# Performance work log

Measured on AMD Instinct MI355X. Metric: run time of the kernel, lower is better.

The kernel has to match this reference:

```python
import jax, jax.numpy as jnp
import numpy as np

N_NODES = 50000
DIM = 64
HEADS = 4
N_EDGES = 800000
NEG_SLOPE = 0.2  # PyG GATConv default


def setup_inputs() -> dict:
    key = jax.random.key(0)
    ks = jax.random.split(key, 8)
    H, C = HEADS, DIM
    embedding = jax.random.normal(ks[0], (N_NODES, DIM), dtype=jnp.float32)
    graph = jax.random.randint(ks[1], (2, N_EDGES), 0, N_NODES, dtype=jnp.int64)
    s = 1.0 / np.sqrt(DIM)
    # GATConv params: shared source/target linear (PyG uses one lin when in_channels is int)
    W = jax.random.normal(ks[2], (DIM, H * C), dtype=jnp.float32) * s
    att_src = jax.random.normal(ks[3], (H, C), dtype=jnp.float32) * s
    att_dst = jax.random.normal(ks[4], (H, C), dtype=jnp.float32) * s
    bias = jnp.zeros((H * C,), dtype=jnp.float32)
    # dense: Linear(dim*heads -> dim)
    dense_w = jax.random.normal(ks[5], (H * C, DIM), dtype=jnp.float32) / np.sqrt(H * C)
    dense_b = jnp.zeros((DIM,), dtype=jnp.float32)
    return {"embedding": embedding, "graph": graph, "W": W, "att_src": att_src,
            "att_dst": att_dst, "bias": bias, "dense_w": dense_w, "dense_b": dense_b}


def reference(embedding, graph, W, att_src, att_dst, bias, dense_w, dense_b):
    N, D = embedding.shape
    H, C = att_src.shape
    # linear projection, per-head view: [N, H, C]
    x = (embedding @ W).reshape(N, H, C)
    # add self loops (PyG default add_self_loops=True)
    ar = jnp.arange(N, dtype=graph.dtype)
    src = jnp.concatenate([graph[0], ar])  # [E+N]
    dst = jnp.concatenate([graph[1], ar])
    # per-node attention logits, gathered per edge
    a_src = jnp.einsum('nhc,hc->nh', x, att_src)  # [N, H]
    a_dst = jnp.einsum('nhc,hc->nh', x, att_dst)
    alpha = jax.nn.leaky_relu(a_src[src] + a_dst[dst], NEG_SLOPE)  # [E, H]
    # segment softmax over destination nodes
    amax = jax.ops.segment_max(alpha, dst, num_segments=N)  # [N, H]
    amax = jnp.where(jnp.isfinite(amax), amax, 0.0)
    ex = jnp.exp(alpha - amax[dst])
    denom = jax.ops.segment_sum(ex, dst, num_segments=N)
    coef = ex / (denom[dst] + 1e-16)  # [E, H]
    # weighted scatter-aggregate of source features
    msg = x[src] * coef[:, :, None]  # [E, H, C]
    agg = jax.ops.segment_sum(msg, dst, num_segments=N)  # [N, H, C]
    gat_out = agg.reshape(N, H * C) + bias  # concat heads + bias
    return gat_out @ dense_w + dense_b  # [N, D]
```

## Files before the change

### kernel.cpp

```cpp
#include <hip/hip_runtime.h>
#include <hip/hip_fp16.h>
#include <cfloat>
#include <cmath>

#define DIM 64
#define HEADS 4
#define NEG 0.2f
#define CAP 64

__device__ __forceinline__ float lrelu(float a) { return a > 0.0f ? a : NEG * a; }

__device__ __forceinline__ unsigned pack_half2(float a, float b) {
    return (unsigned)__half_as_ushort(__float2half(a)) |
           ((unsigned)__half_as_ushort(__float2half(b)) << 16);
}

__global__ __launch_bounds__(256) void prep_kernel(
        const float* __restrict__ W, const float* __restrict__ dw,
        const float* __restrict__ att_s, const float* __restrict__ att_d,
        const float* __restrict__ bias, const float* __restrict__ db,
        const float* __restrict__ emb,
        float* __restrict__ M, float* __restrict__ bvec,
        float* __restrict__ a_src, float* __restrict__ a_dst,
        float* __restrict__ pself, int* __restrict__ cnt, int N) {
    const int b = blockIdx.x, t = threadIdx.x;
    if (b < 64) {
        __shared__ float s_W[256];
        s_W[t] = W[b * 256 + t];
        __syncthreads();
        const int h = t >> 6, j = t & 63;
        float s = 0.f;
        for (int c = 0; c < 64; c++)
            s = fmaf(s_W[h * 64 + c], dw[(h * 64 + c) * 64 + j], s);
        M[b * 256 + t] = s;
    } else if (b == 64) {
        __shared__ float s_p[256];
        const int j = t & 63, kq = t >> 6;
        float p = 0.f;
        for (int k = kq * 64; k < kq * 64 + 64; k++)
            p = fmaf(bias[k], dw[k * 64 + j], p);
        s_p[t] = p;
        __syncthreads();
        if (t < 64)
            bvec[t] = s_p[t] + s_p[64 + t] + s_p[128 + t] + s_p[192 + t] + db[t];
    } else {
        __shared__ float s_e[64 * 68];
        __shared__ float s_vs[256], s_vd[256];
        const int n0 = (b - 65) * 64;
        {
            const int d = t >> 2, h = t & 3;
            const float4* w4 = (const float4*)(W + d * 256 + h * 64);
            const float4* s4 = (const float4*)(att_s + h * 64);
            const float4* d4 = (const float4*)(att_d + h * 64);
            float vs = 0.f, vd = 0.f;
#pragma unroll
            for (int k = 0; k < 16; k++) {
                float4 w = w4[k], as = s4[k], ad = d4[k];
                vs = fmaf(w.x, as.x, fmaf(w.y, as.y, fmaf(w.z, as.z, fmaf(w.w, as.w, vs))));
                vd = fmaf(w.x, ad.x, fmaf(w.y, ad.y, fmaf(w.z, ad.z, fmaf(w.w, ad.w, vd))));
            }
            s_vs[h * 64 + d] = vs;
            s_vd[h * 64 + d] = vd;
        }
#pragma unroll
        for (int r = 0; r < 4; r++) {
            int idx = (r * 256 + t) * 4;
            int i = idx >> 6, d = idx & 63;
            int row = min(n0 + i, N - 1);
            *(float4*)(s_e + i * 68 + d) = *(const float4*)(emb + (size_t)row * 64 + d);
        }
        __syncthreads();
        const int node = t >> 2, h = t & 3;
        const float* er = s_e + node * 68;
        float as = 0.f, ad = 0.f;
#pragma unroll
        for (int g = 0; g < 16; g++) {
            float4 ev = *(const float4*)(er + 4 * g);
            float4 vs = *(const float4*)(s_vs + h * 64 + 4 * g);
            float4 vd = *(const float4*)(s_vd + h * 64 + 4 * g);
            as = fmaf(ev.x, vs.x, fmaf(ev.y, vs.y, fmaf(ev.z, vs.z, fmaf(ev.w, vs.w, as))));
            ad = fmaf(ev.x, vd.x, fmaf(ev.y, vd.y, fmaf(ev.z, vd.z, fmaf(ev.w, vd.w, ad))));
        }
        const int n = n0 + node;
        if (n < N) {
            a_src[(size_t)n * 4 + h] = as;
            a_dst[(size_t)n * 4 + h] = ad;
            pself[(size_t)n * 4 + h] = __expf(lrelu(as + ad));
        }
        if (t < 64 && n0 + t < N) cnt[n0 + t] = 0;
    }
}

__global__ __launch_bounds__(256) void mid_kernel(
        const int* __restrict__ gsrc, const int* __restrict__ gdst,
        const float* __restrict__ a_src, const float* __restrict__ a_dst,
        int* __restrict__ cnt, uint4* __restrict__ rec,
        const float* __restrict__ emb, const float* __restrict__ M,
        unsigned* __restrict__ y32, int E, int N, int FB) {
    __shared__ float s_e[64 * 68];
    const int t = threadIdx.x;

    if ((int)blockIdx.x < FB) {
        const int e0 = (blockIdx.x * 256 + t) * 4;
        if (e0 >= E) return;
        int4 s4, d4;
        if (e0 + 3 < E) {
            s4 = *(const int4*)(gsrc + e0);
            d4 = *(const int4*)(gdst + e0);
        } else {
            int* sp = (int*)&s4; int* dp = (int*)&d4;
            for (int k = 0; k < 4; k++) {
                int e = min(e0 + k, E - 1);
                sp[k] = gsrc[e]; dp[k] = gdst[e];
            }
        }
        const int nk = min(4, E - e0);
#pragma unroll
        for (int k = 0; k < 4; k++) {
            if (k >= nk) break;
            const int s = ((const int*)&s4)[k];
            const int d = ((const int*)&d4)[k];
            float4 as = *(const float4*)(a_src + (size_t)s * 4);
            float4 ad = *(const float4*)(a_dst + (size_t)d * 4);
            uint4 r;
            r.x = (unsigned)s;
            r.y = pack_half2(__expf(lrelu(as.x + ad.x)), __expf(lrelu(as.y + ad.y)));
            r.z = pack_half2(__expf(lrelu(as.z + ad.z)), __expf(lrelu(as.w + ad.w)));
            r.w = 0u;
            int pos = atomicAdd(&cnt[d], 1);
            if (pos < CAP) rec[(size_t)d * CAP + pos] = r;
        }
        return;
    }

    const int l = t & 63;
    const int wq = __builtin_amdgcn_readfirstlane(t >> 6);
    const int n0 = (blockIdx.x - FB) * 64;

#pragma unroll
    for (int r = 0; r < 4; r++) {
        int idx = (r * 256 + t) * 4;
        int i = idx >> 6, d = idx & 63;
        int row = min(n0 + i, N - 1);
        *(float4*)(s_e + i * 68 + d) = *(const float4*)(emb + (size_t)row * 64 + d);
    }
    __syncthreads();

    float4 acc[16];
#pragma unroll
    for (int i = 0; i < 16; i++) acc[i] = make_float4(0.f, 0.f, 0.f, 0.f);

    const float* eb = s_e + wq * 16 * 68;

    for (int g = 0; g < 16; g++) {
        const int d0 = g * 4;
        float4 wv0 = *(const float4*)(M + (d0 + 0) * 256 + 4 * l);
        float4 wv1 = *(const float4*)(M + (d0 + 1) * 256 + 4 * l);
        float4 wv2 = *(const float4*)(M + (d0 + 2) * 256 + 4 * l);
        float4 wv3 = *(const float4*)(M + (d0 + 3) * 256 + 4 * l);
#pragma unroll
        for (int i = 0; i < 16; i++) {
            float4 ev = *(const float4*)(eb + i * 68 + d0);
            acc[i].x = fmaf(ev.x, wv0.x, acc[i].x);
            acc[i].y = fmaf(ev.x, wv0.y, acc[i].y);
            acc[i].z = fmaf(ev.x, wv0.z, acc[i].z);
            acc[i].w = fmaf(ev.x, wv0.w, acc[i].w);
            acc[i].x = fmaf(ev.y, wv1.x, acc[i].x);
            acc[i].y = fmaf(ev.y, wv1.y, acc[i].y);
            acc[i].z = fmaf(ev.y, wv1.z, acc[i].z);
            acc[i].w = fmaf(ev.y, wv1.w, acc[i].w);
            acc[i].x = fmaf(ev.z, wv2.x, acc[i].x);
            acc[i].y = fmaf(ev.z, wv2.y, acc[i].y);
            acc[i].z = fmaf(ev.z, wv2.z, acc[i].z);
            acc[i].w = fmaf(ev.z, wv2.w, acc[i].w);
            acc[i].x = fmaf(ev.w, wv3.x, acc[i].x);
            acc[i].y = fmaf(ev.w, wv3.y, acc[i].y);
            acc[i].z = fmaf(ev.w, wv3.z, acc[i].z);
            acc[i].w = fmaf(ev.w, wv3.w, acc[i].w);
        }
    }

#pragma unroll
    for (int i = 0; i < 16; i++) {
        int n = n0 + wq * 16 + i;
        if (n < N) {
            uint2 u;
            u.x = pack_half2(acc[i].x, acc[i].y);
            u.y = pack_half2(acc[i].z, acc[i].w);
            *(uint2*)(y32 + (size_t)n * 128 + 2 * l) = u;
        }
    }
}

__global__ __launch_bounds__(256) void aggregate_kernel(
        const int* __restrict__ cnt, const uint4* __restrict__ rec,
        const float* __restrict__ pself,
        const unsigned* __restrict__ y32, const float* __restrict__ bvec,
        float* __restrict__ out, int N) {
    const int t = threadIdx.x;
    const int l = t & 63;
    const int dd = blockIdx.x * 4 + (t >> 6);
    if (dd >= N) return;
    const int d = __builtin_amdgcn_readfirstlane(dd);
    const int hl = l >> 4;
    const int deg = min(__builtin_amdgcn_readfirstlane(cnt[d]), CAP);
    const uint4* rb = rec + (size_t)d * CAP;
    const unsigned* yl = y32 + 2 * l;

    float p = pself[(size_t)d * 4 + hl];
    uint2 v = *(const uint2*)(yl + (size_t)d * 128);
    float2 f0 = __half22float2(*(const __half2*)&v.x);
    float2 f1 = __half22float2(*(const __half2*)&v.y);
    float den = p;
    float ax = p * f0.x, ay = p * f0.y, az = p * f1.x, aw = p * f1.y;

#pragma unroll 4
    for (int i = 0; i < deg; i++) {
        const uint4 r = rb[i];
        const unsigned ph = (hl & 2) ? r.z : r.y;
        const unsigned sh = (hl & 1) ? (ph >> 16) : (ph & 0xffffu);
        const float pe = __half2float(__ushort_as_half((unsigned short)sh));
        const uint2 vv = *(const uint2*)(yl + (size_t)r.x * 128);
        float2 g0 = __half22float2(*(const __half2*)&vv.x);
        float2 g1 = __half22float2(*(const __half2*)&vv.y);
        den += pe;
        ax = fmaf(pe, g0.x, ax);
        ay = fmaf(pe, g0.y, ay);
        az = fmaf(pe, g1.x, az);
        aw = fmaf(pe, g1.y, aw);
    }

    const float inv = 1.0f / (den + 1e-16f);
    float rx = ax * inv, ry = ay * inv, rz = az * inv, rw = aw * inv;
    rx += __shfl_xor(rx, 16, 64); ry += __shfl_xor(ry, 16, 64);
    rz += __shfl_xor(rz, 16, 64); rw += __shfl_xor(rw, 16, 64);
    rx += __shfl_xor(rx, 32, 64); ry += __shfl_xor(ry, 32, 64);
    rz += __shfl_xor(rz, 32, 64); rw += __shfl_xor(rw, 32, 64);
    if (l < 16) {
        float4 bv = *(const float4*)(bvec + 4 * l);
        float4 r;
        r.x = rx + bv.x; r.y = ry + bv.y; r.z = rz + bv.z; r.w = rw + bv.w;
        *(float4*)(out + (size_t)dd * 64 + 4 * l) = r;
    }
}

extern "C" void kernel_launch(void* const* d_in, const int* in_sizes, int n_in,
                              void* d_out, int out_size, void* d_ws, size_t ws_size,
                              hipStream_t stream) {
    const float* emb   = (const float*)d_in[0];
    const int*   graph = (const int*)d_in[1];
    const float* W     = (const float*)d_in[2];
    const float* att_s = (const float*)d_in[3];
    const float* att_d = (const float*)d_in[4];
    const float* bias  = (const float*)d_in[5];
    const float* dw    = (const float*)d_in[6];
    const float* db    = (const float*)d_in[7];
    float* out = (float*)d_out;

    const int N = in_sizes[0] / DIM;
    const int E = in_sizes[1] / 2;
    const int* gsrc = graph;
    const int* gdst = graph + E;

    unsigned* y32  = (unsigned*)d_ws;
    uint4* rec     = (uint4*)(y32 + (size_t)N * 128);
    float* a_src   = (float*)(rec + (size_t)N * CAP);
    float* a_dst   = a_src + (size_t)N * 4;
    float* pself   = a_dst + (size_t)N * 4;
    float* M       = pself + (size_t)N * 4;
    float* bvec    = M + 64 * 256;
    int*   cnt     = (int*)(bvec + 64);

    const int quads = (E + 3) / 4;
    const int FB = (quads + 255) / 256;
    const int PB = (N + 63) / 64;

    hipLaunchKernelGGL(prep_kernel, dim3(65 + PB), dim3(256), 0, stream,
                       W, dw, att_s, att_d, bias, db, emb,
                       M, bvec, a_src, a_dst, pself, cnt, N);
    hipLaunchKernelGGL(mid_kernel, dim3(FB + PB), dim3(256), 0, stream,
                       gsrc, gdst, a_src, a_dst, cnt, rec,
                       emb, M, y32, E, N, FB);
    hipLaunchKernelGGL(aggregate_kernel, dim3((N + 3) / 4), dim3(256), 0, stream,
                       cnt, rec, pself, y32, bvec, out, N);
}
```

Baseline: 216.0 us.

## Store only source indices in adjacency and compute edge weights during aggregation

The scatter phase now writes only a 4-byte source index per edge into the per-destination adjacency slots, instead of a 16-byte record holding fp16 exp-weights. The aggregate kernel recomputes exp(leaky_relu(a_src[s]+a_dst[d])) per edge by gathering a_src, and also computes the self-loop weight on the fly, so the pself buffer goes away. This cuts scatter write traffic and adjacency read bandwidth, and lets the aggregate loop load adjacency with int4 vector loads. In exchange it adds one extra scattered a_src gather and an exp per edge per lane.

```diff
diff --git a/kernel.cpp b/kernel.cpp
--- a/kernel.cpp
+++ b/kernel.cpp
@@ -22,7 +22,7 @@
         const float* __restrict__ emb,
         float* __restrict__ M, float* __restrict__ bvec,
         float* __restrict__ a_src, float* __restrict__ a_dst,
-        float* __restrict__ pself, int* __restrict__ cnt, int N) {
+        int* __restrict__ cnt, int N) {
     const int b = blockIdx.x, t = threadIdx.x;
     if (b < 64) {
         __shared__ float s_W[256];
@@ -85,7 +85,6 @@
         if (n < N) {
             a_src[(size_t)n * 4 + h] = as;
             a_dst[(size_t)n * 4 + h] = ad;
-            pself[(size_t)n * 4 + h] = __expf(lrelu(as + ad));
         }
         if (t < 64 && n0 + t < N) cnt[n0 + t] = 0;
     }
@@ -93,8 +92,7 @@
 
 __global__ __launch_bounds__(256) void mid_kernel(
         const int* __restrict__ gsrc, const int* __restrict__ gdst,
-        const float* __restrict__ a_src, const float* __restrict__ a_dst,
-        int* __restrict__ cnt, uint4* __restrict__ rec,
+        int* __restrict__ cnt, int* __restrict__ adj,
         const float* __restrict__ emb, const float* __restrict__ M,
         unsigned* __restrict__ y32, int E, int N, int FB) {
     __shared__ float s_e[64 * 68];
@@ -103,32 +101,23 @@
     if ((int)blockIdx.x < FB) {
         const int e0 = (blockIdx.x * 256 + t) * 4;
         if (e0 >= E) return;
-        int4 s4, d4;
         if (e0 + 3 < E) {
-            s4 = *(const int4*)(gsrc + e0);
-            d4 = *(const int4*)(gdst + e0);
+            const int4 s4 = *(const int4*)(gsrc + e0);
+            const int4 d4 = *(const int4*)(gdst + e0);
+            const int p0 = atomicAdd(&cnt[d4.x], 1);
+            const int p1 = atomicAdd(&cnt[d4.y], 1);
+            const int p2 = atomicAdd(&cnt[d4.z], 1);
+            const int p3 = atomicAdd(&cnt[d4.w], 1);
+            if (p0 < CAP) adj[(size_t)d4.x * CAP + p0] = s4.x;
+            if (p1 < CAP) adj[(size_t)d4.y * CAP + p1] = s4.y;
+            if (p2 < CAP) adj[(size_t)d4.z * CAP + p2] = s4.z;
+            if (p3 < CAP) adj[(size_t)d4.w * CAP + p3] = s4.w;
         } else {
-            int* sp = (int*)&s4; int* dp = (int*)&d4;
-            for (int k = 0; k < 4; k++) {
-                int e = min(e0 + k, E - 1);
-                sp[k] = gsrc[e]; dp[k] = gdst[e];
+            for (int e = e0; e < E; e++) {
+                const int s = gsrc[e], dn = gdst[e];
+                const int pos = atomicAdd(&cnt[dn], 1);
+                if (pos < CAP) adj[(size_t)dn * CAP + pos] = s;
             }
-        }
-        const int nk = min(4, E - e0);
-#pragma unroll
-        for (int k = 0; k < 4; k++) {
-            if (k >= nk) break;
-            const int s = ((const int*)&s4)[k];
-            const int d = ((const int*)&d4)[k];
-            float4 as = *(const float4*)(a_src + (size_t)s * 4);
-            float4 ad = *(const float4*)(a_dst + (size_t)d * 4);
-            uint4 r;
-            r.x = (unsigned)s;
-            r.y = pack_half2(__expf(lrelu(as.x + ad.x)), __expf(lrelu(as.y + ad.y)));
-            r.z = pack_half2(__expf(lrelu(as.z + ad.z)), __expf(lrelu(as.w + ad.w)));
-            r.w = 0u;
-            int pos = atomicAdd(&cnt[d], 1);
-            if (pos < CAP) rec[(size_t)d * CAP + pos] = r;
         }
         return;
     }
@@ -193,8 +182,8 @@
 }
 
 __global__ __launch_bounds__(256) void aggregate_kernel(
-        const int* __restrict__ cnt, const uint4* __restrict__ rec,
-        const float* __restrict__ pself,
+        const int* __restrict__ cnt, const int* __restrict__ adj,
+        const float* __restrict__ a_src, const float* __restrict__ a_dst,
         const unsigned* __restrict__ y32, const float* __restrict__ bvec,
         float* __restrict__ out, int N) {
     const int t = threadIdx.x;
@@ -204,31 +193,39 @@
     const int d = __builtin_amdgcn_readfirstlane(dd);
     const int hl = l >> 4;
     const int deg = min(__builtin_amdgcn_readfirstlane(cnt[d]), CAP);
-    const uint4* rb = rec + (size_t)d * CAP;
+    const int* ab = adj + (size_t)d * CAP;
     const unsigned* yl = y32 + 2 * l;
 
-    float p = pself[(size_t)d * 4 + hl];
+    const float ad = a_dst[(size_t)d * 4 + hl];
+
+    float p = __expf(lrelu(a_src[(size_t)d * 4 + hl] + ad));
     uint2 v = *(const uint2*)(yl + (size_t)d * 128);
     float2 f0 = __half22float2(*(const __half2*)&v.x);
     float2 f1 = __half22float2(*(const __half2*)&v.y);
     float den = p;
     float ax = p * f0.x, ay = p * f0.y, az = p * f1.x, aw = p * f1.y;
 
-#pragma unroll 4
-    for (int i = 0; i < deg; i++) {
-        const uint4 r = rb[i];
-        const unsigned ph = (hl & 2) ? r.z : r.y;
-        const unsigned sh = (hl & 1) ? (ph >> 16) : (ph & 0xffffu);
-        const float pe = __half2float(__ushort_as_half((unsigned short)sh));
-        const uint2 vv = *(const uint2*)(yl + (size_t)r.x * 128);
-        float2 g0 = __half22float2(*(const __half2*)&vv.x);
-        float2 g1 = __half22float2(*(const __half2*)&vv.y);
-        den += pe;
-        ax = fmaf(pe, g0.x, ax);
-        ay = fmaf(pe, g0.y, ay);
-        az = fmaf(pe, g1.x, az);
-        aw = fmaf(pe, g1.y, aw);
-    }
+#define AGG_EDGE(S) {                                                      \
+        const int s_ = (S);                                                \
+        const float as_ = a_src[(size_t)s_ * 4 + hl];                      \
+        const uint2 vv_ = *(const uint2*)(yl + (size_t)s_ * 128);          \
+        const float pe_ = __expf(lrelu(as_ + ad));                         \
+        const float2 g0_ = __half22float2(*(const __half2*)&vv_.x);        \
+        const float2 g1_ = __half22float2(*(const __half2*)&vv_.y);        \
+        den += pe_;                                                        \
+        ax = fmaf(pe_, g0_.x, ax); ay = fmaf(pe_, g0_.y, ay);              \
+        az = fmaf(pe_, g1_.x, az); aw = fmaf(pe_, g1_.y, aw); }
+
+#pragma unroll 1
+    for (int i = 0; i < deg; i += 4) {
+        const int4 a4 = *(const int4*)(ab + i);
+        const int m = deg - i;
+        AGG_EDGE(a4.x);
+        if (m > 1) AGG_EDGE(a4.y);
+        if (m > 2) AGG_EDGE(a4.z);
+        if (m > 3) AGG_EDGE(a4.w);
+    }
+#undef AGG_EDGE
 
     const float inv = 1.0f / (den + 1e-16f);
     float rx = ax * inv, ry = ay * inv, rz = az * inv, rw = aw * inv;
@@ -263,11 +260,10 @@
     const int* gdst = graph + E;
 
     unsigned* y32  = (unsigned*)d_ws;
-    uint4* rec     = (uint4*)(y32 + (size_t)N * 128);
-    float* a_src   = (float*)(rec + (size_t)N * CAP);
+    int* adj       = (int*)(y32 + (size_t)N * 128);
+    float* a_src   = (float*)(adj + (size_t)N * CAP);
     float* a_dst   = a_src + (size_t)N * 4;
-    float* pself   = a_dst + (size_t)N * 4;
-    float* M       = pself + (size_t)N * 4;
+    float* M       = a_dst + (size_t)N * 4;
     float* bvec    = M + 64 * 256;
     int*   cnt     = (int*)(bvec + 64);
 
@@ -277,10 +273,9 @@
 
     hipLaunchKernelGGL(prep_kernel, dim3(65 + PB), dim3(256), 0, stream,
                        W, dw, att_s, att_d, bias, db, emb,
-                       M, bvec, a_src, a_dst, pself, cnt, N);
+                       M, bvec, a_src, a_dst, cnt, N);
     hipLaunchKernelGGL(mid_kernel, dim3(FB + PB), dim3(256), 0, stream,
-                       gsrc, gdst, a_src, a_dst, cnt, rec,
-                       emb, M, y32, E, N, FB);
+                       gsrc, gdst, cnt, adj, emb, M, y32, E, N, FB);
     hipLaunchKernelGGL(aggregate_kernel, dim3((N + 3) / 4), dim3(256), 0, stream,
-                       cnt, rec, pself, y32, bvec, out, N);
-}
+                       cnt, adj, a_src, a_dst, y32, bvec, out, N);
+}
```

Measured after the change: 227.3 us. 5.2% more time.
